# Optimization experiments

Hardware: AMD Instinct MI355X
Metric: run time of the kernel (lower is better)

## Reference

```python
import jax, jax.numpy as jnp
import numpy as np

NUM_GROUPS = 14
GROUP_IN = 9
SHARED_H = 16
SHARED_OUT = 4
SALE_DIM = 1
FINAL_H = 128
ACTION_DIM = 15


def setup_inputs() -> dict:
    key = jax.random.key(0)
    ks = jax.random.split(key, 10)
    B = 262144
    features_2 = jax.random.normal(ks[0], (B, NUM_GROUPS * GROUP_IN), dtype=jnp.float32)
    sale_predictions = jax.random.normal(ks[1], (B, SALE_DIM), dtype=jnp.float32)
    # shared block params (one block, shared across all 14 groups)
    W1 = jax.random.normal(ks[2], (GROUP_IN, SHARED_H), dtype=jnp.float32) / np.sqrt(GROUP_IN)
    b1 = jnp.zeros((SHARED_H,), dtype=jnp.float32)
    W2 = jax.random.normal(ks[3], (SHARED_H, SHARED_OUT), dtype=jnp.float32) / np.sqrt(SHARED_H)
    b2 = jnp.zeros((SHARED_OUT,), dtype=jnp.float32)
    # final block params
    fin_in = SHARED_OUT * NUM_GROUPS + SALE_DIM  # 57
    W3 = jax.random.normal(ks[4], (fin_in, FINAL_H), dtype=jnp.float32) / np.sqrt(fin_in)
    b3 = jnp.zeros((FINAL_H,), dtype=jnp.float32)
    W4 = jax.random.normal(ks[5], (FINAL_H, ACTION_DIM * 2), dtype=jnp.float32) / np.sqrt(FINAL_H)
    b4 = jnp.zeros((ACTION_DIM * 2,), dtype=jnp.float32)
    return {"features_2": features_2, "sale_predictions": sale_predictions,
            "W1": W1, "b1": b1, "W2": W2, "b2": b2,
            "W3": W3, "b3": b3, "W4": W4, "b4": b4}


def reference(features_2, sale_predictions, W1, b1, W2, b2, W3, b3, W4, b4):
    B = features_2.shape[0]
    # [B, 14, 9]: all 14 groups through the SAME shared block, batched as one GEMM
    g = features_2.reshape(B, NUM_GROUPS, GROUP_IN)
    h = jax.nn.relu(jnp.einsum('bgi,ih->bgh', g, W1) + b1)          # [B,14,16]
    s = jax.nn.relu(jnp.einsum('bgh,ho->bgo', h, W2) + b2)          # [B,14,4]
    shared_outputs = s.reshape(B, NUM_GROUPS * SHARED_OUT)          # [B,56]
    combined = jnp.concatenate([shared_outputs, sale_predictions], axis=1)  # [B,57]
    z = jax.nn.relu(combined @ W3 + b3)                             # [B,128]
    out = z @ W4 + b4                                               # [B,30]
    action_mean, action_log_std = jnp.split(out, 2, axis=1)
    action_mean = jnp.tanh(action_mean)
    action_std = jnp.exp(action_log_std)
    return (action_mean, action_std)
```

## Files before the change

### kernel.cpp

```cpp
#include <hip/hip_runtime.h>


typedef float f4v  __attribute__((ext_vector_type(4)));
typedef short s8v  __attribute__((ext_vector_type(8)));
typedef short s4v  __attribute__((ext_vector_type(4)));
typedef _Float16 h2v __attribute__((ext_vector_type(2)));

constexpr int NG = 14, GI = 9, FH = 128, AD = 15;

__device__ __forceinline__ unsigned short f2bf(float f) {
    unsigned u = __builtin_bit_cast(unsigned, f);
    return (unsigned short)((u + 0x7fffu + ((u >> 16) & 1u)) >> 16);
}
__device__ __forceinline__ float bf2f(unsigned short h) {
    return __builtin_bit_cast(float, (unsigned)h << 16);
}
__device__ __forceinline__ f4v load4u(const float* p) {
    f4v v; __builtin_memcpy(&v, p, 16); return v;
}
__device__ __forceinline__ unsigned pkh(float a, float b) {
    return __builtin_bit_cast(unsigned, __builtin_amdgcn_cvt_pkrtz(a, b));
}

__global__ void pack_kernel(const float* __restrict__ W3,
                            const float* __restrict__ W4,
                            const float* __restrict__ W1,
                            const float* __restrict__ b1,
                            const float* __restrict__ W2,
                            unsigned short* __restrict__ pk) {
    unsigned short* W3h = pk;
    unsigned short* W3l = pk + 8192;
    unsigned short* W4h = pk + 16384;
    unsigned short* W4l = pk + 20480;
    unsigned* pk32 = (unsigned*)pk;
    int t = blockIdx.x * 256 + threadIdx.x;
    if (t < 8192) {
        int j = t & 7, l = (t >> 3) & 63, nt = (t >> 9) & 7, kt = t >> 12;
        int k = kt * 32 + (l >> 4) * 8 + j, n = nt * 16 + (l & 15);
        float v = (k < 57) ? W3[k * FH + n] : 0.f;
        unsigned short h = f2bf(v);
        W3h[t] = h;
        W3l[t] = f2bf(v - bf2f(h));
    }
    if (t < 4096) {
        int j = t & 7, l = (t >> 3) & 63, nt = (t >> 9) & 1, kt = t >> 10;
        int k = kt * 32 + (l >> 4) * 8 + j, n = nt * 16 + (l & 15);
        float v = (n < 30) ? W4[k * 30 + n] : 0.f;
        unsigned short h = f2bf(v);
        W4h[t] = h;
        W4l[t] = f2bf(v - bf2f(h));
    }
    if (t < 72) {
        int i = t >> 3, j2 = t & 7;
        pk32[12288 + t] = pkh(W1[i * 16 + 2 * j2], W1[i * 16 + 2 * j2 + 1]);
    }
    if (t < 8)
        pk32[12360 + t] = pkh(b1[2 * t], b1[2 * t + 1]);
    if (t < 32) {
        int j2 = t >> 2, o = t & 3;
        pk32[12368 + t] = pkh(W2[(2 * j2) * 4 + o], W2[(2 * j2 + 1) * 4 + o]);
    }
}

__global__ __launch_bounds__(256, 4) void actor_fused(
    const float* __restrict__ x,
    const float* __restrict__ sale,
    const float* __restrict__ b2,
    const float* __restrict__ b3,
    const float* __restrict__ b4,
    const unsigned short* __restrict__ pk,
    float* __restrict__ om, float* __restrict__ os)
{
    __shared__ unsigned short xz[8192];
    __shared__ unsigned short sh[4096];

    const int tid  = threadIdx.x;
    const int wv   = __builtin_amdgcn_readfirstlane(tid >> 6);
    const int lane = tid & 63;
    const int row0 = blockIdx.x * 64;

    {
        const float* xs = x + (size_t)(row0 + 16 * wv) * (NG * GI);
        unsigned* xw = (unsigned*)(xz + 16 * wv * 126);
        #pragma unroll
        for (int j = 0; j < 8; ++j) {
            int ci = j * 64 + lane;
            if (j < 7 || ci < 504) {
                f4v v = load4u(xs + 4 * ci);
                xw[2 * ci]     = pkh(v[0], v[1]);
                xw[2 * ci + 1] = pkh(v[2], v[3]);
            }
        }
    }
    if (lane < 16) {
        int r = 16 * wv + lane;
        float sv = sale[row0 + r];
        int byt = (r * 128 + 112) ^ ((r & 7) << 4);
        *(unsigned short*)((char*)sh + byt) = f2bf(sv);
        #pragma unroll
        for (int kk = 57; kk < 64; ++kk) {
            int bb = (r * 128 + kk * 2) ^ ((r & 7) << 4);
            *(unsigned short*)((char*)sh + bb) = 0;
        }
    }

    const int r1 = 16 * wv + (lane & 15);
    const int q  = lane >> 4;
    const h2v* w1p = (const h2v*)(pk + 24576);
    const h2v* b1p = (const h2v*)(pk + 24720);
    const h2v* w2p = (const h2v*)(pk + 24736);
    const _Float16* xhp = (const _Float16*)xz;

    auto do_group = [&](int gg) {
        const int hb = r1 * 126 + gg * 9;
        h2v h0 = b1p[0], h1 = b1p[1], h2 = b1p[2], h3 = b1p[3],
            h4 = b1p[4], h5 = b1p[5], h6 = b1p[6], h7 = b1p[7];
        #pragma unroll
        for (int i = 0; i < 9; ++i) {
            _Float16 xs1 = xhp[hb + i];
            h2v xb = (h2v){xs1, xs1};
            const h2v* wr = w1p + i * 8;
            h0 += xb * wr[0]; h1 += xb * wr[1];
            h2 += xb * wr[2]; h3 += xb * wr[3];
            h4 += xb * wr[4]; h5 += xb * wr[5];
            h6 += xb * wr[6]; h7 += xb * wr[7];
        }
        const h2v zz = (h2v)(_Float16)0;
        h0 = __builtin_elementwise_max(h0, zz);
        h1 = __builtin_elementwise_max(h1, zz);
        h2 = __builtin_elementwise_max(h2, zz);
        h3 = __builtin_elementwise_max(h3, zz);
        h4 = __builtin_elementwise_max(h4, zz);
        h5 = __builtin_elementwise_max(h5, zz);
        h6 = __builtin_elementwise_max(h6, zz);
        h7 = __builtin_elementwise_max(h7, zz);
        float sv4[4];
        #pragma unroll
        for (int o = 0; o < 4; ++o) {
            h2v a2 = zz;
            a2 += h0 * w2p[0 * 4 + o];
            a2 += h1 * w2p[1 * 4 + o];
            a2 += h2 * w2p[2 * 4 + o];
            a2 += h3 * w2p[3 * 4 + o];
            a2 += h4 * w2p[4 * 4 + o];
            a2 += h5 * w2p[5 * 4 + o];
            a2 += h6 * w2p[6 * 4 + o];
            a2 += h7 * w2p[7 * 4 + o];
            float s = (float)a2[0] + (float)a2[1] + b2[o];
            sv4[o] = fmaxf(s, 0.f);
        }
        s4v hi = (s4v){(short)f2bf(sv4[0]), (short)f2bf(sv4[1]),
                       (short)f2bf(sv4[2]), (short)f2bf(sv4[3])};
        int byt = (r1 * 128 + gg * 8) ^ ((r1 & 7) << 4);
        *(s4v*)((char*)sh + byt) = hi;
    };
    do_group(q); do_group(q + 4); do_group(q + 8);
    if (q < 2) do_group(q + 12);

    __syncthreads();

    const s8v* W3hv = (const s8v*)pk;
    const s8v* W3lv = (const s8v*)(pk + 8192);
    s8v bh[2][2], bl[2][2];
    #pragma unroll
    for (int kt = 0; kt < 2; ++kt)
        #pragma unroll
        for (int ntl = 0; ntl < 2; ++ntl) {
            int nt = 2 * wv + ntl;
            bh[kt][ntl] = W3hv[(kt * 8 + nt) * 64 + lane];
            bl[kt][ntl] = W3lv[(kt * 8 + nt) * 64 + lane];
        }
    f4v acc[4][2];
    #pragma unroll
    for (int ntl = 0; ntl < 2; ++ntl) {
        float bv = b3[32 * wv + ntl * 16 + (lane & 15)];
        #pragma unroll
        for (int mt = 0; mt < 4; ++mt) acc[mt][ntl] = (f4v){bv, bv, bv, bv};
    }
    #pragma unroll
    for (int kt = 0; kt < 2; ++kt) {
        s8v ah[4];
        #pragma unroll
        for (int mt = 0; mt < 4; ++mt) {
            int rr = mt * 16 + (lane & 15);
            int byt = (rr * 128 + kt * 64 + (lane >> 4) * 16) ^ ((rr & 7) << 4);
            ah[mt] = *(const s8v*)((char*)sh + byt);
        }
        #pragma unroll
        for (int mt = 0; mt < 4; ++mt)
            #pragma unroll
            for (int ntl = 0; ntl < 2; ++ntl) {
                acc[mt][ntl] = __builtin_amdgcn_mfma_f32_16x16x32_bf16(ah[mt], bh[kt][ntl], acc[mt][ntl], 0, 0, 0);
                acc[mt][ntl] = __builtin_amdgcn_mfma_f32_16x16x32_bf16(ah[mt], bl[kt][ntl], acc[mt][ntl], 0, 0, 0);
            }
    }
    #pragma unroll
    for (int mt = 0; mt < 4; ++mt)
        #pragma unroll
        for (int ntl = 0; ntl < 2; ++ntl) {
            const int col = 32 * wv + ntl * 16 + (lane & 15);
            #pragma unroll
            for (int i = 0; i < 4; ++i) {
                int rowl = mt * 16 + (lane >> 4) * 4 + i;
                float v = fmaxf(acc[mt][ntl][i], 0.f);
                int byt = (rowl * 256 + col * 2) ^ ((rowl & 7) << 4);
                *(unsigned short*)((char*)xz + byt) = f2bf(v);
            }
        }

    __syncthreads();

    const s8v* W4hv = (const s8v*)(pk + 16384);
    const s8v* W4lv = (const s8v*)(pk + 20480);
    const int mq   = __builtin_amdgcn_readfirstlane(wv >> 1);
    const int nq   = __builtin_amdgcn_readfirstlane(wv & 1);
    const int ocol = nq * 16 + (lane & 15);
    const float b4i = (ocol < 30) ? b4[ocol] : 0.f;

    f4v oa0 = (f4v){b4i, b4i, b4i, b4i};
    f4v oa1 = oa0;
    #pragma unroll
    for (int kt = 0; kt < 4; ++kt) {
        s8v wh = W4hv[(kt * 2 + nq) * 64 + lane];
        s8v wl = W4lv[(kt * 2 + nq) * 64 + lane];
        int rr0 = mq * 32 + (lane & 15);
        int by0 = (rr0 * 256 + kt * 64 + (lane >> 4) * 16) ^ ((rr0 & 7) << 4);
        s8v z0 = *(const s8v*)((char*)xz + by0);
        oa0 = __builtin_amdgcn_mfma_f32_16x16x32_bf16(z0, wh, oa0, 0, 0, 0);
        oa0 = __builtin_amdgcn_mfma_f32_16x16x32_bf16(z0, wl, oa0, 0, 0, 0);
        int rr1 = rr0 + 16;
        int by1 = (rr1 * 256 + kt * 64 + (lane >> 4) * 16) ^ ((rr1 & 7) << 4);
        s8v z1 = *(const s8v*)((char*)xz + by1);
        oa1 = __builtin_amdgcn_mfma_f32_16x16x32_bf16(z1, wh, oa1, 0, 0, 0);
        oa1 = __builtin_amdgcn_mfma_f32_16x16x32_bf16(z1, wl, oa1, 0, 0, 0);
    }
    #pragma unroll
    for (int mi = 0; mi < 2; ++mi) {
        f4v oa = mi ? oa1 : oa0;
        #pragma unroll
        for (int i = 0; i < 4; ++i) {
            int grow = row0 + mq * 32 + mi * 16 + (lane >> 4) * 4 + i;
            float v = oa[i];
            if (ocol < AD) {
                float tc = fminf(fmaxf(v, -20.f), 20.f);
                float e = __expf(2.f * tc);
                om[(size_t)grow * AD + ocol] = (e - 1.f) / (e + 1.f);
            } else if (ocol < 2 * AD) {
                os[(size_t)grow * AD + (ocol - AD)] = __expf(v);
            }
        }
    }
}

extern "C" void kernel_launch(void* const* d_in, const int* in_sizes, int n_in,
                              void* d_out, int out_size, void* d_ws, size_t ws_size,
                              hipStream_t stream) {
    const float* x    = (const float*)d_in[0];
    const float* sale = (const float*)d_in[1];
    const float* W1   = (const float*)d_in[2];
    const float* b1   = (const float*)d_in[3];
    const float* W2   = (const float*)d_in[4];
    const float* b2   = (const float*)d_in[5];
    const float* W3   = (const float*)d_in[6];
    const float* b3   = (const float*)d_in[7];
    const float* W4   = (const float*)d_in[8];
    const float* b4   = (const float*)d_in[9];

    int B = in_sizes[1];
    float* om = (float*)d_out;
    float* os = om + (size_t)B * AD;
    unsigned short* pk = (unsigned short*)d_ws;

    pack_kernel<<<32, 256, 0, stream>>>(W3, W4, W1, b1, W2, pk);
    actor_fused<<<B / 64, 256, 0, stream>>>(x, sale, b2, b3, b4, pk, om, os);
}
```

Baseline: 54.57 us.

## Use packed bf16 converts and transposed LDS reads for the final GEMM operand

Replaces the software round-to-nearest bf16 conversion with the hardware v_cvt_pk_bf16_f32 instruction. The hidden-layer activations are now written to LDS as packed 4-element column chunks instead of scalar 2-byte stores, and read back with ds_read_b64_tr_b16 transposing loads. The W4 fragments are hoisted out of the loop. This is meant to cut LDS store instructions and conversion ALU work, at the cost of a custom LDS layout that must exactly match the MFMA operand ordering.

```diff
diff --git a/kernel.cpp b/kernel.cpp
--- a/kernel.cpp
+++ b/kernel.cpp
@@ -3,8 +3,9 @@
 
 typedef float f4v  __attribute__((ext_vector_type(4)));
 typedef short s8v  __attribute__((ext_vector_type(8)));
-typedef short s4v  __attribute__((ext_vector_type(4)));
 typedef _Float16 h2v __attribute__((ext_vector_type(2)));
+typedef unsigned u2v __attribute__((ext_vector_type(2)));
+typedef unsigned u4v __attribute__((ext_vector_type(4)));
 
 constexpr int NG = 14, GI = 9, FH = 128, AD = 15;
 
@@ -20,6 +21,11 @@
 }
 __device__ __forceinline__ unsigned pkh(float a, float b) {
     return __builtin_bit_cast(unsigned, __builtin_amdgcn_cvt_pkrtz(a, b));
+}
+__device__ __forceinline__ unsigned pkbf(float a, float b) {
+    unsigned r;
+    asm("v_cvt_pk_bf16_f32 %0, %1, %2" : "=v"(r) : "v"(a), "v"(b));
+    return r;
 }
 
 __global__ void pack_kernel(const float* __restrict__ W3,
@@ -149,10 +155,10 @@
             float s = (float)a2[0] + (float)a2[1] + b2[o];
             sv4[o] = fmaxf(s, 0.f);
         }
-        s4v hi = (s4v){(short)f2bf(sv4[0]), (short)f2bf(sv4[1]),
-                       (short)f2bf(sv4[2]), (short)f2bf(sv4[3])};
+        unsigned p01 = pkbf(sv4[0], sv4[1]);
+        unsigned p23 = pkbf(sv4[2], sv4[3]);
         int byt = (r1 * 128 + gg * 8) ^ ((r1 & 7) << 4);
-        *(s4v*)((char*)sh + byt) = hi;
+        *(u2v*)((char*)sh + byt) = (u2v){p01, p23};
     };
     do_group(q); do_group(q + 4); do_group(q + 8);
     if (q < 2) do_group(q + 12);
@@ -198,14 +204,15 @@
     for (int mt = 0; mt < 4; ++mt)
         #pragma unroll
         for (int ntl = 0; ntl < 2; ++ntl) {
-            const int col = 32 * wv + ntl * 16 + (lane & 15);
-            #pragma unroll
-            for (int i = 0; i < 4; ++i) {
-                int rowl = mt * 16 + (lane >> 4) * 4 + i;
-                float v = fmaxf(acc[mt][ntl][i], 0.f);
-                int byt = (rowl * 256 + col * 2) ^ ((rowl & 7) << 4);
-                *(unsigned short*)((char*)xz + byt) = f2bf(v);
-            }
+            int kk  = ntl * 16 + (lane & 15);
+            int tau = (kk & 4) ? 4 + (kk >> 3) : (kk >> 3);
+            int eidx = mt * 2048 + wv * 512 + tau * 64 + (kk & 3) * 16
+                     + ((lane >> 4) << 2);
+            float v0 = fmaxf(acc[mt][ntl][0], 0.f);
+            float v1 = fmaxf(acc[mt][ntl][1], 0.f);
+            float v2 = fmaxf(acc[mt][ntl][2], 0.f);
+            float v3 = fmaxf(acc[mt][ntl][3], 0.f);
+            *(u2v*)(xz + eidx) = (u2v){pkbf(v0, v1), pkbf(v2, v3)};
         }
 
     __syncthreads();
@@ -217,22 +224,39 @@
     const int ocol = nq * 16 + (lane & 15);
     const float b4i = (ocol < 30) ? b4[ocol] : 0.f;
 
+    s8v wh[4], wl[4];
+    #pragma unroll
+    for (int kt = 0; kt < 4; ++kt) {
+        wh[kt] = W4hv[(kt * 2 + nq) * 64 + lane];
+        wl[kt] = W4lv[(kt * 2 + nq) * 64 + lane];
+    }
+    unsigned base = (unsigned)(size_t)&xz[0] + (unsigned)(2 * mq) * 4096u
+                  + (unsigned)(lane * 8);
+    u2v f0[4][2], f1[4][2];
+    #pragma unroll
+    for (int c = 0; c < 4; ++c) {
+        unsigned a0 = base + c * 1024;
+        unsigned a1 = a0 + 4096;
+        asm volatile("ds_read_b64_tr_b16 %0, %1" : "=v"(f0[c][0]) : "v"(a0));
+        asm volatile("ds_read_b64_tr_b16 %0, %1 offset:512" : "=v"(f0[c][1]) : "v"(a0));
+        asm volatile("ds_read_b64_tr_b16 %0, %1" : "=v"(f1[c][0]) : "v"(a1));
+        asm volatile("ds_read_b64_tr_b16 %0, %1 offset:512" : "=v"(f1[c][1]) : "v"(a1));
+    }
+    asm volatile("s_waitcnt lgkmcnt(0)" ::: "memory");
+    __builtin_amdgcn_sched_barrier(0);
+
     f4v oa0 = (f4v){b4i, b4i, b4i, b4i};
     f4v oa1 = oa0;
     #pragma unroll
     for (int kt = 0; kt < 4; ++kt) {
-        s8v wh = W4hv[(kt * 2 + nq) * 64 + lane];
-        s8v wl = W4lv[(kt * 2 + nq) * 64 + lane];
-        int rr0 = mq * 32 + (lane & 15);
-        int by0 = (rr0 * 256 + kt * 64 + (lane >> 4) * 16) ^ ((rr0 & 7) << 4);
-        s8v z0 = *(const s8v*)((char*)xz + by0);
-        oa0 = __builtin_amdgcn_mfma_f32_16x16x32_bf16(z0, wh, oa0, 0, 0, 0);
-        oa0 = __builtin_amdgcn_mfma_f32_16x16x32_bf16(z0, wl, oa0, 0, 0, 0);
-        int rr1 = rr0 + 16;
-        int by1 = (rr1 * 256 + kt * 64 + (lane >> 4) * 16) ^ ((rr1 & 7) << 4);
-        s8v z1 = *(const s8v*)((char*)xz + by1);
-        oa1 = __builtin_amdgcn_mfma_f32_16x16x32_bf16(z1, wh, oa1, 0, 0, 0);
-        oa1 = __builtin_amdgcn_mfma_f32_16x16x32_bf16(z1, wl, oa1, 0, 0, 0);
+        s8v z0 = __builtin_bit_cast(s8v,
+            (u4v){f0[kt][0][0], f0[kt][0][1], f0[kt][1][0], f0[kt][1][1]});
+        s8v z1 = __builtin_bit_cast(s8v,
+            (u4v){f1[kt][0][0], f1[kt][0][1], f1[kt][1][0], f1[kt][1][1]});
+        oa0 = __builtin_amdgcn_mfma_f32_16x16x32_bf16(z0, wh[kt], oa0, 0, 0, 0);
+        oa0 = __builtin_amdgcn_mfma_f32_16x16x32_bf16(z0, wl[kt], oa0, 0, 0, 0);
+        oa1 = __builtin_amdgcn_mfma_f32_16x16x32_bf16(z1, wh[kt], oa1, 0, 0, 0);
+        oa1 = __builtin_amdgcn_mfma_f32_16x16x32_bf16(z1, wl[kt], oa1, 0, 0, 0);
     }
     #pragma unroll
     for (int mi = 0; mi < 2; ++mi) {
```

After: 50.01 us. -8.4%, faster.
